# Kernel tuning notes

Hardware: AMD Instinct MI355X
Metric: run time of the kernel (lower is better)

Reference implementation:

```python
import jax, jax.numpy as jnp
import numpy as np

IN_FEATURES = 1
OUT_FEATURES = 64
LATENT = 16
N_HARMONICS = 16
N_EIG = 2
BATCH = 16384
COEFFS_SIZE = (IN_FEATURES + 1) * OUT_FEATURES * N_HARMONICS * N_EIG  # 4096


def setup_inputs() -> dict:
    key = jax.random.key(0)
    ks = jax.random.split(key, 6)
    x = jax.random.normal(ks[0], (BATCH, IN_FEATURES + 1 + LATENT), dtype=jnp.float32)
    # CoeffDecoder params: fc1 (latent -> coeffs_size), fc2 (coeffs_size -> coeffs_size)
    fc1_w = jax.random.normal(ks[1], (COEFFS_SIZE, LATENT), dtype=jnp.float32) * (1.0 / np.sqrt(LATENT))
    fc1_b = jax.random.normal(ks[2], (COEFFS_SIZE,), dtype=jnp.float32) * 0.01
    fc2_w = jax.random.normal(ks[3], (COEFFS_SIZE, COEFFS_SIZE), dtype=jnp.float32) * (1.0 / np.sqrt(COEFFS_SIZE))
    fc2_b = jax.random.normal(ks[4], (COEFFS_SIZE,), dtype=jnp.float32) * 0.01
    dilation = jnp.ones((1,), dtype=jnp.float32)
    shift = jnp.zeros((1,), dtype=jnp.float32)
    return {"x": x, "fc1_w": fc1_w, "fc1_b": fc1_b, "fc2_w": fc2_w, "fc2_b": fc2_b,
            "dilation": dilation, "shift": shift}


def reference(x, fc1_w, fc1_b, fc2_w, fc2_b, dilation, shift):
    B = x.shape[0]
    s = x[-1, IN_FEATURES]                         # scalar depth/time channel
    inp = x[:, :IN_FEATURES]                       # [B, 1]
    z = x[:, -LATENT:]                             # [B, latent]
    # CoeffDecoder: 2-layer MLP
    h = jax.nn.relu(z @ fc1_w.T + fc1_b)           # [B, coeffs_size]
    coeffs = (h @ fc2_w.T + fc2_b).reshape(B, (IN_FEATURES + 1) * OUT_FEATURES, N_EIG * N_HARMONICS)
    # Fourier basis. torch.linspace(0, H, H) includes endpoint H.
    n_range = jnp.linspace(0.0, N_HARMONICS, N_HARMONICS).astype(x.dtype)
    arg = s * dilation[0] + shift[0]
    # B matrix is block [diag(cos); diag(sin)] -> X.sum(2) == coeffs @ concat(cos, sin)
    basis = jnp.concatenate([jnp.cos(arg * n_range), jnp.sin(arg * n_range)])  # [2H]
    w = coeffs @ basis                             # [B, (in+1)*out]
    weight = w[:, :IN_FEATURES * OUT_FEATURES]     # [B, out] (in_features == 1)
    bias = w[:, IN_FEATURES * OUT_FEATURES:(IN_FEATURES + 1) * OUT_FEATURES]
    # bmm([B,1,1], [B,1,out]) == scalar input * per-sample weight row
    weighted = inp * weight                        # [B, out]
    return weighted + bias
```

## Files before the change

### kernel.cpp

```cpp
#include <hip/hip_runtime.h>
#include <hip/hip_bf16.h>
#include <math.h>

#define BATCH  16384
#define XDIM   18
#define LATENT 16
#define NM     128
#define KDIM   4096
#define OUTF   64
#define KB     32
#define BM     64

typedef short s16x8 __attribute__((ext_vector_type(8)));
typedef float f32x16 __attribute__((ext_vector_type(16)));

__device__ __forceinline__ unsigned short f2bf(float f) {
    union { float f; unsigned u; } v; v.f = f;
    return (unsigned short)((v.u + 0x7FFFu + ((v.u >> 16) & 1u)) >> 16);
}
__device__ __forceinline__ unsigned pack_bf2(float a, float b) {
    __hip_bfloat162 h = __float22bfloat162_rn(make_float2(a, b));
    return *(unsigned*)&h;
}
__device__ __forceinline__ int swap23(int m) {
    return (m & ~12) | ((m & 4) << 1) | ((m & 8) >> 1);
}

__global__ __launch_bounds__(128) void precompute_kernel(
    const float* __restrict__ x, const float* __restrict__ fc1_w,
    const float* __restrict__ fc1_b, const float* __restrict__ fc2_w,
    const float* __restrict__ fc2_b, const float* __restrict__ dil,
    const float* __restrict__ shf, unsigned short* __restrict__ wfrag,
    unsigned short* __restrict__ f1frag, float* __restrict__ bh,
    float* __restrict__ beff)
{
    const int tid = threadIdx.x;
    const int bid = blockIdx.x;
    if (bid < 512) {
        __shared__ float basis[KB];
        __shared__ float bred[32];
        if (tid < KB) {
            const float s   = x[(size_t)(BATCH - 1) * XDIM + 1];
            const float arg = s * dil[0] + shf[0];
            const float n   = 16.0f * (float)(tid & 15) / 15.0f;
            const float a   = arg * n;
            basis[tid] = (tid < 16) ? cosf(a) : sinf(a);
        }
        __syncthreads();
        const int m  = bid >> 2, kq = bid & 3;
        const int k8 = kq * 128 + tid;
        const int k  = k8 * 8;
        float acc[8] = {0.f,0.f,0.f,0.f,0.f,0.f,0.f,0.f};
        const float* src = fc2_w + (size_t)m * KB * KDIM + k;
        #pragma unroll 4
        for (int kb = 0; kb < KB; ++kb) {
            const float wgt = basis[kb];
            const float4 a = *(const float4*)(src + (size_t)kb * KDIM);
            const float4 b = *(const float4*)(src + (size_t)kb * KDIM + 4);
            acc[0] = fmaf(wgt, a.x, acc[0]); acc[1] = fmaf(wgt, a.y, acc[1]);
            acc[2] = fmaf(wgt, a.z, acc[2]); acc[3] = fmaf(wgt, a.w, acc[3]);
            acc[4] = fmaf(wgt, b.x, acc[4]); acc[5] = fmaf(wgt, b.y, acc[5]);
            acc[6] = fmaf(wgt, b.z, acc[6]); acc[7] = fmaf(wgt, b.w, acc[7]);
        }
        const int ct = m >> 5, coln = m & 31;
        const int kc = k8 >> 1, kg = k8 & 1;
        const int lane = kg * 32 + coln;
        unsigned short t[8];
        #pragma unroll
        for (int i = 0; i < 8; ++i) t[i] = f2bf(acc[i]);
        *(uint4*)(wfrag + ((size_t)(kc * 4 + ct) * 64 + lane) * 8) = *(const uint4*)t;
        if (kq == 0 && tid < 32) bred[tid] = basis[tid] * fc2_b[m * KB + tid];
        __syncthreads();
        if (kq == 0 && tid == 0) {
            float s = 0.f;
            #pragma unroll
            for (int i = 0; i < 32; ++i) s += bred[i];
            beff[m] = s;
        }
    } else if (bid < 576) {
        const int slot = (bid - 512) * 128 + tid;
        const int lane = slot & 63;
        const int jt   = slot >> 6;
        const int j    = jt * 32 + swap23(lane & 31);
        const int kg   = lane >> 5;
        const float* src = fc1_w + (size_t)j * LATENT + kg * 8;
        const float4 a = *(const float4*)(src);
        const float4 b = *(const float4*)(src + 4);
        unsigned short t[8];
        t[0]=f2bf(a.x); t[1]=f2bf(a.y); t[2]=f2bf(a.z); t[3]=f2bf(a.w);
        t[4]=f2bf(b.x); t[5]=f2bf(b.y); t[6]=f2bf(b.z); t[7]=f2bf(b.w);
        *(uint4*)(f1frag + (size_t)slot * 8) = *(const uint4*)t;
    } else {
        const int jt = tid;
        #pragma unroll
        for (int mp = 0; mp < 32; ++mp) {
            const int lg = mp >> 4, r = mp & 15;
            const int crow = (r & 3) + 8 * (r >> 2) + 4 * lg;
            bh[jt * 32 + mp] = fc1_b[jt * 32 + swap23(crow)];
        }
    }
}

__global__ __launch_bounds__(1024, 4) void fused_kernel(
    const float* __restrict__ x,
    const unsigned short* __restrict__ wfrag,
    const unsigned short* __restrict__ f1frag,
    const float* __restrict__ bh,
    const float* __restrict__ beff, float* __restrict__ out)
{
    __shared__ float bhs[128 * 32];
    __shared__ float wfull[BM * NM];

    const int tid = threadIdx.x;
    const int w   = tid >> 6, l = tid & 63;
    const int l31 = l & 31,  lg = l >> 5;
    const int row0 = blockIdx.x * BM;
    const int rt = w & 1, ctp = (w >> 1) & 1, ks = w >> 2;

    ((float4*)bhs)[tid] = ((const float4*)bh)[tid];

    s16x8 zfrag;
    {
        const float* zp = x + (size_t)(row0 + rt * 32 + l31) * XDIM + 2 + lg * 8;
        #pragma unroll
        for (int q = 0; q < 4; ++q) {
            const float2 t = *(const float2*)(zp + 2 * q);
            ((unsigned*)&zfrag)[q] = pack_bf2(t.x, t.y);
        }
    }

    f32x16 acc0, acc1;
    #pragma unroll
    for (int i = 0; i < 16; ++i) { acc0[i] = 0.0f; acc1[i] = 0.0f; }

    __syncthreads();

    const unsigned short* fvp = f1frag + ((size_t)(ks * 32) * 64 + l) * 8;
    const float*          bhp = bhs + (ks * 32) * 32 + lg * 16;
    const unsigned short* bp  = wfrag + ((size_t)(2 * (ks * 32)) * 4 + 2 * ctp) * 512 + l * 8;

    auto compute = [&](const uint4& fv, const s16x8& B0, const s16x8& B1,
                       const s16x8& B2, const s16x8& B3, const float* bq) {
        const float4 c0 = *(const float4*)(bq);
        const float4 c1 = *(const float4*)(bq + 4);
        const float4 c2 = *(const float4*)(bq + 8);
        const float4 c3 = *(const float4*)(bq + 12);
        f32x16 hc;
        hc[0]=c0.x;  hc[1]=c0.y;  hc[2]=c0.z;  hc[3]=c0.w;
        hc[4]=c1.x;  hc[5]=c1.y;  hc[6]=c1.z;  hc[7]=c1.w;
        hc[8]=c2.x;  hc[9]=c2.y;  hc[10]=c2.z; hc[11]=c2.w;
        hc[12]=c3.x; hc[13]=c3.y; hc[14]=c3.z; hc[15]=c3.w;
        hc = __builtin_amdgcn_mfma_f32_32x32x16_bf16(*(const s16x8*)&fv, zfrag, hc, 0, 0, 0);
        unsigned a0[4], a1[4];
        #pragma unroll
        for (int q = 0; q < 4; ++q) {
            a0[q] = pack_bf2(fmaxf(hc[2*q],   0.f), fmaxf(hc[2*q+1],   0.f));
            a1[q] = pack_bf2(fmaxf(hc[8+2*q], 0.f), fmaxf(hc[8+2*q+1], 0.f));
        }
        acc0 = __builtin_amdgcn_mfma_f32_32x32x16_bf16(*(const s16x8*)a0, B0, acc0, 0, 0, 0);
        acc1 = __builtin_amdgcn_mfma_f32_32x32x16_bf16(*(const s16x8*)a0, B1, acc1, 0, 0, 0);
        acc0 = __builtin_amdgcn_mfma_f32_32x32x16_bf16(*(const s16x8*)a1, B2, acc0, 0, 0, 0);
        acc1 = __builtin_amdgcn_mfma_f32_32x32x16_bf16(*(const s16x8*)a1, B3, acc1, 0, 0, 0);
    };

    uint4 fvA = *(const uint4*)(fvp);
    s16x8 B0A = *(const s16x8*)(bp);
    s16x8 B1A = *(const s16x8*)(bp + 512);
    s16x8 B2A = *(const s16x8*)(bp + 2048);
    s16x8 B3A = *(const s16x8*)(bp + 2560);

    for (int t = 0; t < 32; t += 2) {
        const uint4 fvB = *(const uint4*)(fvp + 512);
        const s16x8 B0B = *(const s16x8*)(bp + 4096);
        const s16x8 B1B = *(const s16x8*)(bp + 4096 + 512);
        const s16x8 B2B = *(const s16x8*)(bp + 4096 + 2048);
        const s16x8 B3B = *(const s16x8*)(bp + 4096 + 2560);
        compute(fvA, B0A, B1A, B2A, B3A, bhp);

        fvA = *(const uint4*)(fvp + 1024);
        B0A = *(const s16x8*)(bp + 8192);
        B1A = *(const s16x8*)(bp + 8192 + 512);
        B2A = *(const s16x8*)(bp + 8192 + 2048);
        B3A = *(const s16x8*)(bp + 8192 + 2560);
        compute(fvB, B0B, B1B, B2B, B3B, bhp + 32);

        fvp += 1024; bp += 8192; bhp += 64;
    }

    #pragma unroll 1
    for (int p = 0; p < 4; ++p) {
        if (ks == p) {
            const float be0 = beff[(2 * ctp) * 32 + l31];
            const float be1 = beff[(2 * ctp + 1) * 32 + l31];
            #pragma unroll
            for (int r = 0; r < 16; ++r) {
                const int rowl = (r & 3) + 8 * (r >> 2) + 4 * lg;
                const int idx  = (rt * 32 + rowl) * NM + (2 * ctp) * 32 + l31;
                if (p == 0) {
                    wfull[idx]      = acc0[r] + be0;
                    wfull[idx + 32] = acc1[r] + be1;
                } else {
                    wfull[idx]      += acc0[r];
                    wfull[idx + 32] += acc1[r];
                }
            }
        }
        __syncthreads();
    }

    {
        const int o = tid & 63, rg = tid >> 6;
        #pragma unroll
        for (int i = 0; i < 4; ++i) {
            const int r = rg * 4 + i;
            const float inp = x[(size_t)(row0 + r) * XDIM];
            out[(size_t)(row0 + r) * OUTF + o] =
                fmaf(inp, wfull[r * NM + o], wfull[r * NM + OUTF + o]);
        }
    }
}

extern "C" void kernel_launch(void* const* d_in, const int* in_sizes, int n_in,
                              void* d_out, int out_size, void* d_ws, size_t ws_size,
                              hipStream_t stream) {
    const float* x     = (const float*)d_in[0];
    const float* fc1_w = (const float*)d_in[1];
    const float* fc1_b = (const float*)d_in[2];
    const float* fc2_w = (const float*)d_in[3];
    const float* fc2_b = (const float*)d_in[4];
    const float* dil   = (const float*)d_in[5];
    const float* shf   = (const float*)d_in[6];
    float* out = (float*)d_out;

    unsigned short* wfrag  = (unsigned short*)d_ws;
    unsigned short* f1frag = wfrag + 524288;
    float*          beff   = (float*)(f1frag + 65536);
    float*          bh     = beff + NM;

    precompute_kernel<<<577, 128, 0, stream>>>(x, fc1_w, fc1_b, fc2_w, fc2_b,
                                               dil, shf, wfrag, f1frag, bh, beff);
    fused_kernel<<<BATCH / BM, 1024, 0, stream>>>(x, wfrag, f1frag, bh, beff, out);
}
```

Measured before the change: 48.69 us.

## Assign waves one column tile across both row tiles to halve B-fragment loads

Each wave now covers a single 32-column output tile for both 32-row tiles, instead of one row tile and two column tiles. Each B fragment loaded from the fc2 weights is reused for two row tiles, so per-wave global B loads drop by half. In exchange, the fc1 MFMA and ReLU/pack step runs for both row tiles in every wave, which duplicates first-layer work and raises register use. The software prefetch is also restructured so both A and B buffers are loaded one step ahead, which reads slightly past the last tile on the final iteration.

```diff
diff --git a/kernel.cpp b/kernel.cpp
--- a/kernel.cpp
+++ b/kernel.cpp
@@ -115,17 +115,20 @@
     const int w   = tid >> 6, l = tid & 63;
     const int l31 = l & 31,  lg = l >> 5;
     const int row0 = blockIdx.x * BM;
-    const int rt = w & 1, ctp = (w >> 1) & 1, ks = w >> 2;
+    const int ct = w & 3, ks = w >> 2;
 
     ((float4*)bhs)[tid] = ((const float4*)bh)[tid];
 
-    s16x8 zfrag;
+    s16x8 zfrag0, zfrag1;
     {
-        const float* zp = x + (size_t)(row0 + rt * 32 + l31) * XDIM + 2 + lg * 8;
+        const float* zp0 = x + (size_t)(row0 + l31) * XDIM + 2 + lg * 8;
+        const float* zp1 = x + (size_t)(row0 + 32 + l31) * XDIM + 2 + lg * 8;
         #pragma unroll
         for (int q = 0; q < 4; ++q) {
-            const float2 t = *(const float2*)(zp + 2 * q);
-            ((unsigned*)&zfrag)[q] = pack_bf2(t.x, t.y);
+            const float2 t0 = *(const float2*)(zp0 + 2 * q);
+            const float2 t1 = *(const float2*)(zp1 + 2 * q);
+            ((unsigned*)&zfrag0)[q] = pack_bf2(t0.x, t0.y);
+            ((unsigned*)&zfrag1)[q] = pack_bf2(t1.x, t1.y);
         }
     }
 
@@ -137,10 +140,10 @@
 
     const unsigned short* fvp = f1frag + ((size_t)(ks * 32) * 64 + l) * 8;
     const float*          bhp = bhs + (ks * 32) * 32 + lg * 16;
-    const unsigned short* bp  = wfrag + ((size_t)(2 * (ks * 32)) * 4 + 2 * ctp) * 512 + l * 8;
+    const unsigned short* bp  = wfrag + ((size_t)(2 * (ks * 32)) * 4 + ct) * 512 + l * 8;
 
     auto compute = [&](const uint4& fv, const s16x8& B0, const s16x8& B1,
-                       const s16x8& B2, const s16x8& B3, const float* bq) {
+                       const float* bq) {
         const float4 c0 = *(const float4*)(bq);
         const float4 c1 = *(const float4*)(bq + 4);
         const float4 c2 = *(const float4*)(bq + 8);
@@ -150,39 +153,43 @@
         hc[4]=c1.x;  hc[5]=c1.y;  hc[6]=c1.z;  hc[7]=c1.w;
         hc[8]=c2.x;  hc[9]=c2.y;  hc[10]=c2.z; hc[11]=c2.w;
         hc[12]=c3.x; hc[13]=c3.y; hc[14]=c3.z; hc[15]=c3.w;
-        hc = __builtin_amdgcn_mfma_f32_32x32x16_bf16(*(const s16x8*)&fv, zfrag, hc, 0, 0, 0);
-        unsigned a0[4], a1[4];
+        f32x16 h0 = __builtin_amdgcn_mfma_f32_32x32x16_bf16(*(const s16x8*)&fv, zfrag0, hc, 0, 0, 0);
+        unsigned a00[4], a10[4];
         #pragma unroll
         for (int q = 0; q < 4; ++q) {
-            a0[q] = pack_bf2(fmaxf(hc[2*q],   0.f), fmaxf(hc[2*q+1],   0.f));
-            a1[q] = pack_bf2(fmaxf(hc[8+2*q], 0.f), fmaxf(hc[8+2*q+1], 0.f));
-        }
-        acc0 = __builtin_amdgcn_mfma_f32_32x32x16_bf16(*(const s16x8*)a0, B0, acc0, 0, 0, 0);
-        acc1 = __builtin_amdgcn_mfma_f32_32x32x16_bf16(*(const s16x8*)a0, B1, acc1, 0, 0, 0);
-        acc0 = __builtin_amdgcn_mfma_f32_32x32x16_bf16(*(const s16x8*)a1, B2, acc0, 0, 0, 0);
-        acc1 = __builtin_amdgcn_mfma_f32_32x32x16_bf16(*(const s16x8*)a1, B3, acc1, 0, 0, 0);
+            a00[q] = pack_bf2(fmaxf(h0[2*q],   0.f), fmaxf(h0[2*q+1],   0.f));
+            a10[q] = pack_bf2(fmaxf(h0[8+2*q], 0.f), fmaxf(h0[8+2*q+1], 0.f));
+        }
+        f32x16 h1 = __builtin_amdgcn_mfma_f32_32x32x16_bf16(*(const s16x8*)&fv, zfrag1, hc, 0, 0, 0);
+        unsigned a01[4], a11[4];
+        #pragma unroll
+        for (int q = 0; q < 4; ++q) {
+            a01[q] = pack_bf2(fmaxf(h1[2*q],   0.f), fmaxf(h1[2*q+1],   0.f));
+            a11[q] = pack_bf2(fmaxf(h1[8+2*q], 0.f), fmaxf(h1[8+2*q+1], 0.f));
+        }
+        acc0 = __builtin_amdgcn_mfma_f32_32x32x16_bf16(*(const s16x8*)a00, B0, acc0, 0, 0, 0);
+        acc1 = __builtin_amdgcn_mfma_f32_32x32x16_bf16(*(const s16x8*)a01, B0, acc1, 0, 0, 0);
+        acc0 = __builtin_amdgcn_mfma_f32_32x32x16_bf16(*(const s16x8*)a10, B1, acc0, 0, 0, 0);
+        acc1 = __builtin_amdgcn_mfma_f32_32x32x16_bf16(*(const s16x8*)a11, B1, acc1, 0, 0, 0);
     };
 
     uint4 fvA = *(const uint4*)(fvp);
     s16x8 B0A = *(const s16x8*)(bp);
-    s16x8 B1A = *(const s16x8*)(bp + 512);
-    s16x8 B2A = *(const s16x8*)(bp + 2048);
-    s16x8 B3A = *(const s16x8*)(bp + 2560);
+    s16x8 B1A = *(const s16x8*)(bp + 2048);
+    uint4 fvB = *(const uint4*)(fvp + 512);
+    s16x8 B0B = *(const s16x8*)(bp + 4096);
+    s16x8 B1B = *(const s16x8*)(bp + 4096 + 2048);
 
     for (int t = 0; t < 32; t += 2) {
-        const uint4 fvB = *(const uint4*)(fvp + 512);
-        const s16x8 B0B = *(const s16x8*)(bp + 4096);
-        const s16x8 B1B = *(const s16x8*)(bp + 4096 + 512);
-        const s16x8 B2B = *(const s16x8*)(bp + 4096 + 2048);
-        const s16x8 B3B = *(const s16x8*)(bp + 4096 + 2560);
-        compute(fvA, B0A, B1A, B2A, B3A, bhp);
-
+        compute(fvA, B0A, B1A, bhp);
         fvA = *(const uint4*)(fvp + 1024);
         B0A = *(const s16x8*)(bp + 8192);
-        B1A = *(const s16x8*)(bp + 8192 + 512);
-        B2A = *(const s16x8*)(bp + 8192 + 2048);
-        B3A = *(const s16x8*)(bp + 8192 + 2560);
-        compute(fvB, B0B, B1B, B2B, B3B, bhp + 32);
+        B1A = *(const s16x8*)(bp + 8192 + 2048);
+
+        compute(fvB, B0B, B1B, bhp + 32);
+        fvB = *(const uint4*)(fvp + 1536);
+        B0B = *(const s16x8*)(bp + 12288);
+        B1B = *(const s16x8*)(bp + 12288 + 2048);
 
         fvp += 1024; bp += 8192; bhp += 64;
     }
@@ -190,18 +197,17 @@
     #pragma unroll 1
     for (int p = 0; p < 4; ++p) {
         if (ks == p) {
-            const float be0 = beff[(2 * ctp) * 32 + l31];
-            const float be1 = beff[(2 * ctp + 1) * 32 + l31];
+            const float be = beff[ct * 32 + l31];
             #pragma unroll
             for (int r = 0; r < 16; ++r) {
                 const int rowl = (r & 3) + 8 * (r >> 2) + 4 * lg;
-                const int idx  = (rt * 32 + rowl) * NM + (2 * ctp) * 32 + l31;
+                const int idx  = rowl * NM + ct * 32 + l31;
                 if (p == 0) {
-                    wfull[idx]      = acc0[r] + be0;
-                    wfull[idx + 32] = acc1[r] + be1;
+                    wfull[idx]             = acc0[r] + be;
+                    wfull[idx + 32 * NM]   = acc1[r] + be;
                 } else {
-                    wfull[idx]      += acc0[r];
-                    wfull[idx + 32] += acc1[r];
+                    wfull[idx]           += acc0[r];
+                    wfull[idx + 32 * NM] += acc1[r];
                 }
             }
         }
```

Result: slower. 63.99 us (+31.4%).

## Software-pipeline fc1 MFMA one step ahead of fc2 MFMAs and hoist prefetch before barrier

Applied to the files above, without the earlier changes.

The main loop is restructured so the fc1 hidden-tile MFMA for the next k-step is issued before the fc2 MFMAs that consume the current tile. This breaks the dependency between the hidden MFMA, the ReLU/pack, and the fc2 MFMAs within a step. The initial fragment loads are moved ahead of the __syncthreads so global latency overlaps the LDS bias staging. Prefetch now runs two steps ahead, and the LDS bias buffer is padded with zeros so the final look-ahead read stays in bounds. The cost is more live registers (extra fragment sets plus two hidden accumulators) under launch_bounds(1024,4), which may cause spills.

```diff
diff --git a/kernel.cpp b/kernel.cpp
--- a/kernel.cpp
+++ b/kernel.cpp
@@ -108,7 +108,7 @@
     const float* __restrict__ bh,
     const float* __restrict__ beff, float* __restrict__ out)
 {
-    __shared__ float bhs[128 * 32];
+    __shared__ float bhs[132 * 32];
     __shared__ float wfull[BM * NM];
 
     const int tid = threadIdx.x;
@@ -118,6 +118,7 @@
     const int rt = w & 1, ctp = (w >> 1) & 1, ks = w >> 2;
 
     ((float4*)bhs)[tid] = ((const float4*)bh)[tid];
+    if (tid < 32) ((float4*)bhs)[1024 + tid] = make_float4(0.f, 0.f, 0.f, 0.f);
 
     s16x8 zfrag;
     {
@@ -133,14 +134,25 @@
     #pragma unroll
     for (int i = 0; i < 16; ++i) { acc0[i] = 0.0f; acc1[i] = 0.0f; }
 
+    const unsigned short* fvp = f1frag + ((size_t)(ks * 32) * 64 + l) * 8;
+    const unsigned short* bp  = wfrag + ((size_t)(2 * (ks * 32)) * 4 + 2 * ctp) * 512 + l * 8;
+
+    const uint4 fv0 = *(const uint4*)(fvp);
+    uint4 fvO = *(const uint4*)(fvp + 512);
+    uint4 fvE = *(const uint4*)(fvp + 1024);
+    s16x8 B0E = *(const s16x8*)(bp);
+    s16x8 B1E = *(const s16x8*)(bp + 512);
+    s16x8 B2E = *(const s16x8*)(bp + 2048);
+    s16x8 B3E = *(const s16x8*)(bp + 2560);
+    s16x8 B0O = *(const s16x8*)(bp + 4096);
+    s16x8 B1O = *(const s16x8*)(bp + 4096 + 512);
+    s16x8 B2O = *(const s16x8*)(bp + 4096 + 2048);
+    s16x8 B3O = *(const s16x8*)(bp + 4096 + 2560);
+
     __syncthreads();
-
-    const unsigned short* fvp = f1frag + ((size_t)(ks * 32) * 64 + l) * 8;
-    const float*          bhp = bhs + (ks * 32) * 32 + lg * 16;
-    const unsigned short* bp  = wfrag + ((size_t)(2 * (ks * 32)) * 4 + 2 * ctp) * 512 + l * 8;
-
-    auto compute = [&](const uint4& fv, const s16x8& B0, const s16x8& B1,
-                       const s16x8& B2, const s16x8& B3, const float* bq) {
+    const float* bhp = bhs + (ks * 32) * 32 + lg * 16;
+
+    auto hinit = [&](const float* bq) -> f32x16 {
         const float4 c0 = *(const float4*)(bq);
         const float4 c1 = *(const float4*)(bq + 4);
         const float4 c2 = *(const float4*)(bq + 8);
@@ -150,39 +162,53 @@
         hc[4]=c1.x;  hc[5]=c1.y;  hc[6]=c1.z;  hc[7]=c1.w;
         hc[8]=c2.x;  hc[9]=c2.y;  hc[10]=c2.z; hc[11]=c2.w;
         hc[12]=c3.x; hc[13]=c3.y; hc[14]=c3.z; hc[15]=c3.w;
-        hc = __builtin_amdgcn_mfma_f32_32x32x16_bf16(*(const s16x8*)&fv, zfrag, hc, 0, 0, 0);
-        unsigned a0[4], a1[4];
-        #pragma unroll
-        for (int q = 0; q < 4; ++q) {
-            a0[q] = pack_bf2(fmaxf(hc[2*q],   0.f), fmaxf(hc[2*q+1],   0.f));
-            a1[q] = pack_bf2(fmaxf(hc[8+2*q], 0.f), fmaxf(hc[8+2*q+1], 0.f));
-        }
-        acc0 = __builtin_amdgcn_mfma_f32_32x32x16_bf16(*(const s16x8*)a0, B0, acc0, 0, 0, 0);
-        acc1 = __builtin_amdgcn_mfma_f32_32x32x16_bf16(*(const s16x8*)a0, B1, acc1, 0, 0, 0);
-        acc0 = __builtin_amdgcn_mfma_f32_32x32x16_bf16(*(const s16x8*)a1, B2, acc0, 0, 0, 0);
-        acc1 = __builtin_amdgcn_mfma_f32_32x32x16_bf16(*(const s16x8*)a1, B3, acc1, 0, 0, 0);
+        return hc;
     };
 
-    uint4 fvA = *(const uint4*)(fvp);
-    s16x8 B0A = *(const s16x8*)(bp);
-    s16x8 B1A = *(const s16x8*)(bp + 512);
-    s16x8 B2A = *(const s16x8*)(bp + 2048);
-    s16x8 B3A = *(const s16x8*)(bp + 2560);
+    f32x16 hcA = __builtin_amdgcn_mfma_f32_32x32x16_bf16(
+        *(const s16x8*)&fv0, zfrag, hinit(bhp), 0, 0, 0);
+    f32x16 hcB;
 
     for (int t = 0; t < 32; t += 2) {
-        const uint4 fvB = *(const uint4*)(fvp + 512);
-        const s16x8 B0B = *(const s16x8*)(bp + 4096);
-        const s16x8 B1B = *(const s16x8*)(bp + 4096 + 512);
-        const s16x8 B2B = *(const s16x8*)(bp + 4096 + 2048);
-        const s16x8 B3B = *(const s16x8*)(bp + 4096 + 2560);
-        compute(fvA, B0A, B1A, B2A, B3A, bhp);
-
-        fvA = *(const uint4*)(fvp + 1024);
-        B0A = *(const s16x8*)(bp + 8192);
-        B1A = *(const s16x8*)(bp + 8192 + 512);
-        B2A = *(const s16x8*)(bp + 8192 + 2048);
-        B3A = *(const s16x8*)(bp + 8192 + 2560);
-        compute(fvB, B0B, B1B, B2B, B3B, bhp + 32);
+        {
+            unsigned p0[4], p1[4];
+            #pragma unroll
+            for (int q = 0; q < 4; ++q) {
+                p0[q] = pack_bf2(fmaxf(hcA[2*q],   0.f), fmaxf(hcA[2*q+1],   0.f));
+                p1[q] = pack_bf2(fmaxf(hcA[8+2*q], 0.f), fmaxf(hcA[8+2*q+1], 0.f));
+            }
+            acc0 = __builtin_amdgcn_mfma_f32_32x32x16_bf16(*(const s16x8*)p0, B0E, acc0, 0, 0, 0);
+            acc1 = __builtin_amdgcn_mfma_f32_32x32x16_bf16(*(const s16x8*)p0, B1E, acc1, 0, 0, 0);
+            acc0 = __builtin_amdgcn_mfma_f32_32x32x16_bf16(*(const s16x8*)p1, B2E, acc0, 0, 0, 0);
+            acc1 = __builtin_amdgcn_mfma_f32_32x32x16_bf16(*(const s16x8*)p1, B3E, acc1, 0, 0, 0);
+        }
+        hcB = __builtin_amdgcn_mfma_f32_32x32x16_bf16(
+            *(const s16x8*)&fvO, zfrag, hinit(bhp + 32), 0, 0, 0);
+        fvO = *(const uint4*)(fvp + 1536);
+        B0E = *(const s16x8*)(bp + 8192);
+        B1E = *(const s16x8*)(bp + 8192 + 512);
+        B2E = *(const s16x8*)(bp + 8192 + 2048);
+        B3E = *(const s16x8*)(bp + 8192 + 2560);
+
+        {
+            unsigned p0[4], p1[4];
+            #pragma unroll
+            for (int q = 0; q < 4; ++q) {
+                p0[q] = pack_bf2(fmaxf(hcB[2*q],   0.f), fmaxf(hcB[2*q+1],   0.f));
+                p1[q] = pack_bf2(fmaxf(hcB[8+2*q], 0.f), fmaxf(hcB[8+2*q+1], 0.f));
+            }
+            acc0 = __builtin_amdgcn_mfma_f32_32x32x16_bf16(*(const s16x8*)p0, B0O, acc0, 0, 0, 0);
+            acc1 = __builtin_amdgcn_mfma_f32_32x32x16_bf16(*(const s16x8*)p0, B1O, acc1, 0, 0, 0);
+            acc0 = __builtin_amdgcn_mfma_f32_32x32x16_bf16(*(const s16x8*)p1, B2O, acc0, 0, 0, 0);
+            acc1 = __builtin_amdgcn_mfma_f32_32x32x16_bf16(*(const s16x8*)p1, B3O, acc1, 0, 0, 0);
+        }
+        hcA = __builtin_amdgcn_mfma_f32_32x32x16_bf16(
+            *(const s16x8*)&fvE, zfrag, hinit(bhp + 64), 0, 0, 0);
+        fvE = *(const uint4*)(fvp + 2048);
+        B0O = *(const s16x8*)(bp + 12288);
+        B1O = *(const s16x8*)(bp + 12288 + 512);
+        B2O = *(const s16x8*)(bp + 12288 + 2048);
+        B3O = *(const s16x8*)(bp + 12288 + 2560);
 
         fvp += 1024; bp += 8192; bhp += 64;
     }
```

Result: no change. 48.09 us (-1.3%).

## Stream fc2 weight fragments through an LDS ring via global_load_lds

Applied to the files above, without the earlier changes.

Replaces per-wave direct global loads of the fc2 B-fragments with asynchronous global_load_lds DMA into a 4-deep shared-memory ring, so the fragment loads are spread across waves. It also software-pipelines the fc1 MFMA one step ahead of the fc2 MFMAs and prefetches the f1 fragments four steps ahead. The intent is to hide global-memory latency and cut redundant VGPR loads. In exchange it adds a block-wide barrier every iteration and needs about 145 KB of dynamic LDS, which limits the kernel to one 1024-thread block per CU. It also reuses the ring memory as wfull after a final sync.

```diff
diff --git a/kernel.cpp b/kernel.cpp
--- a/kernel.cpp
+++ b/kernel.cpp
@@ -10,6 +10,8 @@
 #define OUTF   64
 #define KB     32
 #define BM     64
+
+#define LDS_BYTES 147968
 
 typedef short s16x8 __attribute__((ext_vector_type(8)));
 typedef float f32x16 __attribute__((ext_vector_type(16)));
@@ -108,16 +110,21 @@
     const float* __restrict__ bh,
     const float* __restrict__ beff, float* __restrict__ out)
 {
-    __shared__ float bhs[128 * 32];
-    __shared__ float wfull[BM * NM];
+    extern __shared__ char smem[];
+    unsigned short* ring = (unsigned short*)smem;
+    float* bhs   = (float*)(smem + 131072);
+    float* wfull = (float*)smem;
 
     const int tid = threadIdx.x;
     const int w   = tid >> 6, l = tid & 63;
     const int l31 = l & 31,  lg = l >> 5;
     const int row0 = blockIdx.x * BM;
-    const int rt = w & 1, ctp = (w >> 1) & 1, ks = w >> 2;
+    const int ks = w >> 2, wi = w & 3;
+    const int rt = wi & 1, ctp = wi >> 1;
+    const int jt0 = ks * 32;
 
     ((float4*)bhs)[tid] = ((const float4*)bh)[tid];
+    if (tid < 32) ((float4*)bhs)[1024 + tid] = make_float4(0.f, 0.f, 0.f, 0.f);
 
     s16x8 zfrag;
     {
@@ -133,14 +140,22 @@
     #pragma unroll
     for (int i = 0; i < 16; ++i) { acc0[i] = 0.0f; acc1[i] = 0.0f; }
 
-    __syncthreads();
-
-    const unsigned short* fvp = f1frag + ((size_t)(ks * 32) * 64 + l) * 8;
-    const float*          bhp = bhs + (ks * 32) * 32 + lg * 16;
-    const unsigned short* bp  = wfrag + ((size_t)(2 * (ks * 32)) * 4 + 2 * ctp) * 512 + l * 8;
-
-    auto compute = [&](const uint4& fv, const s16x8& B0, const s16x8& B1,
-                       const s16x8& B2, const s16x8& B3, const float* bq) {
+    auto dma = [&](int t) {
+        const int jt = jt0 + t;
+        const unsigned short* s0 = wfrag + ((size_t)(2 * jt) * 4 + wi) * 512 + l * 8;
+        unsigned short* d = ring + ((size_t)(ks * 4 + (t & 3)) * 8 + 2 * wi) * 512;
+        __builtin_amdgcn_global_load_lds(
+            (const __attribute__((address_space(1))) unsigned*)s0,
+            (__attribute__((address_space(3))) unsigned*)d, 16, 0, 0);
+        __builtin_amdgcn_global_load_lds(
+            (const __attribute__((address_space(1))) unsigned*)(s0 + 4 * 512),
+            (__attribute__((address_space(3))) unsigned*)(d + 512), 16, 0, 0);
+    };
+    auto fvld = [&](int t) -> uint4 {
+        return *(const uint4*)(f1frag + ((size_t)(jt0 + t) * 64 + l) * 8);
+    };
+    auto hinit = [&](int t) -> f32x16 {
+        const float* bq = bhs + (jt0 + t) * 32 + lg * 16;
         const float4 c0 = *(const float4*)(bq);
         const float4 c1 = *(const float4*)(bq + 4);
         const float4 c2 = *(const float4*)(bq + 8);
@@ -150,42 +165,56 @@
         hc[4]=c1.x;  hc[5]=c1.y;  hc[6]=c1.z;  hc[7]=c1.w;
         hc[8]=c2.x;  hc[9]=c2.y;  hc[10]=c2.z; hc[11]=c2.w;
         hc[12]=c3.x; hc[13]=c3.y; hc[14]=c3.z; hc[15]=c3.w;
-        hc = __builtin_amdgcn_mfma_f32_32x32x16_bf16(*(const s16x8*)&fv, zfrag, hc, 0, 0, 0);
-        unsigned a0[4], a1[4];
+        return hc;
+    };
+
+    __syncthreads();
+    const uint4 fv0 = fvld(0);
+    f32x16 hc = __builtin_amdgcn_mfma_f32_32x32x16_bf16(
+        *(const s16x8*)&fv0, zfrag, hinit(0), 0, 0, 0);
+    dma(0);
+    uint4 F1 = fvld(1);
+    dma(1);
+    uint4 F2 = fvld(2);
+    uint4 F3 = fvld(3);
+    uint4 F0;
+
+    auto body = [&](int t, uint4& F_use, uint4& F_fill) {
+        asm volatile("s_waitcnt vmcnt(4)" ::: "memory");
+        __builtin_amdgcn_s_barrier();
+        __builtin_amdgcn_sched_barrier(0);
+        const unsigned short* sb = ring + ((size_t)(ks * 4 + (t & 3)) * 8 + 4 * ctp) * 512 + l * 8;
+        const s16x8 Ba = *(const s16x8*)(sb);
+        const s16x8 Bb = *(const s16x8*)(sb + 512);
+        const s16x8 Bc = *(const s16x8*)(sb + 1024);
+        const s16x8 Bd = *(const s16x8*)(sb + 1536);
+        dma(t + 2);
+        F_fill = fvld(t + 4);
+        unsigned p0[4], p1[4];
         #pragma unroll
         for (int q = 0; q < 4; ++q) {
-            a0[q] = pack_bf2(fmaxf(hc[2*q],   0.f), fmaxf(hc[2*q+1],   0.f));
-            a1[q] = pack_bf2(fmaxf(hc[8+2*q], 0.f), fmaxf(hc[8+2*q+1], 0.f));
-        }
-        acc0 = __builtin_amdgcn_mfma_f32_32x32x16_bf16(*(const s16x8*)a0, B0, acc0, 0, 0, 0);
-        acc1 = __builtin_amdgcn_mfma_f32_32x32x16_bf16(*(const s16x8*)a0, B1, acc1, 0, 0, 0);
-        acc0 = __builtin_amdgcn_mfma_f32_32x32x16_bf16(*(const s16x8*)a1, B2, acc0, 0, 0, 0);
-        acc1 = __builtin_amdgcn_mfma_f32_32x32x16_bf16(*(const s16x8*)a1, B3, acc1, 0, 0, 0);
-    };
-
-    uint4 fvA = *(const uint4*)(fvp);
-    s16x8 B0A = *(const s16x8*)(bp);
-    s16x8 B1A = *(const s16x8*)(bp + 512);
-    s16x8 B2A = *(const s16x8*)(bp + 2048);
-    s16x8 B3A = *(const s16x8*)(bp + 2560);
-
-    for (int t = 0; t < 32; t += 2) {
-        const uint4 fvB = *(const uint4*)(fvp + 512);
-        const s16x8 B0B = *(const s16x8*)(bp + 4096);
-        const s16x8 B1B = *(const s16x8*)(bp + 4096 + 512);
-        const s16x8 B2B = *(const s16x8*)(bp + 4096 + 2048);
-        const s16x8 B3B = *(const s16x8*)(bp + 4096 + 2560);
-        compute(fvA, B0A, B1A, B2A, B3A, bhp);
-
-        fvA = *(const uint4*)(fvp + 1024);
-        B0A = *(const s16x8*)(bp + 8192);
-        B1A = *(const s16x8*)(bp + 8192 + 512);
-        B2A = *(const s16x8*)(bp + 8192 + 2048);
-        B3A = *(const s16x8*)(bp + 8192 + 2560);
-        compute(fvB, B0B, B1B, B2B, B3B, bhp + 32);
-
-        fvp += 1024; bp += 8192; bhp += 64;
-    }
+            p0[q] = pack_bf2(fmaxf(hc[2*q],   0.f), fmaxf(hc[2*q+1],   0.f));
+            p1[q] = pack_bf2(fmaxf(hc[8+2*q], 0.f), fmaxf(hc[8+2*q+1], 0.f));
+        }
+        hc = __builtin_amdgcn_mfma_f32_32x32x16_bf16(*(const s16x8*)&F_use, zfrag,
+                                                     hinit(t + 1), 0, 0, 0);
+        acc0 = __builtin_amdgcn_mfma_f32_32x32x16_bf16(*(const s16x8*)p0, Ba, acc0, 0, 0, 0);
+        acc0 = __builtin_amdgcn_mfma_f32_32x32x16_bf16(*(const s16x8*)p1, Bb, acc0, 0, 0, 0);
+        acc1 = __builtin_amdgcn_mfma_f32_32x32x16_bf16(*(const s16x8*)p0, Bc, acc1, 0, 0, 0);
+        acc1 = __builtin_amdgcn_mfma_f32_32x32x16_bf16(*(const s16x8*)p1, Bd, acc1, 0, 0, 0);
+    };
+
+    #pragma unroll 1
+    for (int o = 0; o < 8; ++o) {
+        const int t = o * 4;
+        body(t + 0, F1, F0);
+        body(t + 1, F2, F1);
+        body(t + 2, F3, F2);
+        body(t + 3, F0, F3);
+    }
+
+    asm volatile("s_waitcnt vmcnt(0) lgkmcnt(0)" ::: "memory");
+    __syncthreads();
 
     #pragma unroll 1
     for (int p = 0; p < 4; ++p) {
@@ -237,7 +266,11 @@
     float*          beff   = (float*)(f1frag + 65536);
     float*          bh     = beff + NM;
 
+    hipFuncSetAttribute((const void*)fused_kernel,
+                        hipFuncAttributeMaxDynamicSharedMemorySize, LDS_BYTES);
+
     precompute_kernel<<<577, 128, 0, stream>>>(x, fc1_w, fc1_b, fc2_w, fc2_b,
                                                dil, shf, wfrag, f1frag, bh, beff);
-    fused_kernel<<<BATCH / BM, 1024, 0, stream>>>(x, wfrag, f1frag, bh, beff, out);
-}
+    fused_kernel<<<BATCH / BM, 1024, LDS_BYTES, stream>>>(x, wfrag, f1frag, bh,
+                                                          beff, out);
+}
```

New measurement: 49.12 us. About the same (+0.9%).
